# Kernel optimization log

Measured on AMD Instinct MI355X. Metric: run time of the kernel, lower is better.

The kernel has to match this reference:

```python
import jax, jax.numpy as jnp
import numpy as np

INPUT_DIM = 512
KEY_DIM = 256
VOCAB = 10000
MAX_LEN = 300


def setup_inputs() -> dict:
    key = jax.random.key(0)
    ks = jax.random.split(key, 20)
    s = 0.05
    B, S, D, K, V = 32, 196, INPUT_DIM, KEY_DIM, VOCAB
    inp = {
        'x': jax.random.normal(ks[0], (B, S, D), jnp.float32),
        'emb': jax.random.normal(ks[1], (V, D), jnp.float32) * s,
        'Wk': jax.random.normal(ks[2], (K, D), jnp.float32) * s,
        'bk': jnp.zeros((K,), jnp.float32),
        'Wv': jax.random.normal(ks[3], (K, D), jnp.float32) * s,
        'bv': jnp.zeros((K,), jnp.float32),
        'Wq': jax.random.normal(ks[4], (K, D), jnp.float32) * s,
        'bq': jnp.zeros((K,), jnp.float32),
        'Wp': jax.random.normal(ks[5], (V, D + K), jnp.float32) * s,
        'bp': jnp.zeros((V,), jnp.float32),
        # LSTM cell 0: input = concat(embed, context) -> D + K
        'Wih0': jax.random.normal(ks[6], (4 * D, D + K), jnp.float32) * s,
        'Whh0': jax.random.normal(ks[7], (4 * D, D), jnp.float32) * s,
        'bih0': jnp.zeros((4 * D,), jnp.float32),
        'bhh0': jnp.zeros((4 * D,), jnp.float32),
        # LSTM cell 1: input = hidden of cell 0 -> D
        'Wih1': jax.random.normal(ks[8], (4 * D, D), jnp.float32) * s,
        'Whh1': jax.random.normal(ks[9], (4 * D, D), jnp.float32) * s,
        'bih1': jnp.zeros((4 * D,), jnp.float32),
        'bhh1': jnp.zeros((4 * D,), jnp.float32),
    }
    return inp


def _lstm_cell(inp, h, c, Wih, Whh, bih, bhh):
    # torch LSTMCell gate order: i, f, g, o
    gates = inp @ Wih.T + bih + h @ Whh.T + bhh
    i, f, g, o = jnp.split(gates, 4, axis=-1)
    c_new = jax.nn.sigmoid(f) * c + jax.nn.sigmoid(i) * jnp.tanh(g)
    h_new = jax.nn.sigmoid(o) * jnp.tanh(c_new)
    return h_new, c_new


def reference(x, emb, Wk, bk, Wv, bv, Wq, bq, Wp, bp,
              Wih0, Whh0, bih0, bhh0, Wih1, Whh1, bih1, bhh1):
    B = x.shape[0]
    D = Whh0.shape[1]
    K = Wk.shape[0]
    scale = 1.0 / jnp.sqrt(jnp.asarray(K, x.dtype))
    keys = x @ Wk.T + bk      # (B, S, K)
    values = x @ Wv.T + bv    # (B, S, K)

    tok0 = jnp.zeros((B,), jnp.int32)           # argmax of zeros(B,1) == 0
    ctx0 = jnp.zeros((B, K), x.dtype)
    h0 = jnp.zeros((B, D), x.dtype)
    c0 = jnp.zeros((B, D), x.dtype)
    h1 = jnp.zeros((B, D), x.dtype)
    c1 = jnp.zeros((B, D), x.dtype)

    def step(carry, _):
        tok, ctx, h0, c0, h1, c1 = carry
        embed = jnp.concatenate([emb[tok], ctx], axis=1)   # (B, D+K)
        h0, c0 = _lstm_cell(embed, h0, c0, Wih0, Whh0, bih0, bhh0)
        h1, c1 = _lstm_cell(h0, h1, c1, Wih1, Whh1, bih1, bhh1)
        q = h1 @ Wq.T + bq                                  # (B, K)
        energy = jnp.einsum('bsk,bk->bs', keys, q) * scale  # (B, S)
        attn = jax.nn.softmax(energy, axis=-1)
        ctx = jnp.einsum('bs,bsk->bk', attn, values)        # (B, K)
        out = jnp.concatenate([h1, ctx], axis=1)            # (B, D+K)
        pred = out @ Wp.T + bp                              # (B, V)
        tok = jnp.argmax(pred, axis=-1).astype(jnp.int32)
        return (tok, ctx, h0, c0, h1, c1), pred

    _, preds = jax.lax.scan(step, (tok0, ctx0, h0, c0, h1, c1), None, length=MAX_LEN)
    return jnp.transpose(preds, (1, 0, 2))  # (B, MAX_LEN, V)
```

## Files before the change

kernel.cpp:

```cpp
#include <hip/hip_runtime.h>
#include <math.h>


typedef unsigned long long u64;

#define NS 196
#define ND 512
#define NK 256
#define NV 10000
#define NT 300
#define NBLK 256
#define NTHR 512
#define SCOPE __HIP_MEMORY_SCOPE_AGENT

__device__ __forceinline__ float sigm(float x) { return 1.0f / (1.0f + expf(-x)); }

__device__ __forceinline__ float aldf(const float* p) {
  return __hip_atomic_load(p, __ATOMIC_RELAXED, SCOPE);
}
__device__ __forceinline__ void astf(float* p, float v) {
  __hip_atomic_store(p, v, __ATOMIC_RELAXED, SCOPE);
}
__device__ __forceinline__ u64 aldu(const u64* p) {
  return __hip_atomic_load(p, __ATOMIC_RELAXED, SCOPE);
}
__device__ __forceinline__ void astu(u64* p, u64 v) {
  __hip_atomic_store(p, v, __ATOMIC_RELAXED, SCOPE);
}

__device__ __forceinline__ u64 packmax(float x, int v) {
  unsigned u = __float_as_uint(x);
  u = (u & 0x80000000u) ? ~u : (u | 0x80000000u);
  return ((u64)u << 32) | (u64)(0xFFFFFFFFu - (unsigned)v);
}

__device__ __forceinline__ int eslot(int b, int k4) {
  return b * 32 + ((k4 & ~7) | ((k4 ^ b) & 7));
}

__device__ __forceinline__ void gbar(unsigned* bar, int bid, unsigned ep, bool fenced) {
  __syncthreads();
  if (threadIdx.x == 0) {
    if (fenced) __threadfence();
    asm volatile("s_waitcnt vmcnt(0)" ::: "memory");
    const int g = bid & 7;
    const unsigned old = __hip_atomic_fetch_add(&bar[g * 32], 1u, __ATOMIC_RELAXED, SCOPE);
    if (old == ep * 32u - 1u) {
      const unsigned r = __hip_atomic_fetch_add(&bar[512], 1u, __ATOMIC_RELAXED, SCOPE);
      if (r == ep * 8u - 1u) {
#pragma unroll
        for (int i = 0; i < 8; ++i)
          __hip_atomic_store(&bar[256 + i * 32], ep, __ATOMIC_RELAXED, SCOPE);
      }
    }
    while (__hip_atomic_load(&bar[256 + g * 32], __ATOMIC_RELAXED, SCOPE) < ep)
      __builtin_amdgcn_s_sleep(2);
    if (fenced) __threadfence();
  }
  __syncthreads();
}

__global__ __launch_bounds__(256) void k_zbar(unsigned* bar) {
  const int i = blockIdx.x * 256 + threadIdx.x;
  if (i < 1024) bar[i] = 0u;
}

struct Params {
  const float *x, *emb, *Wk, *bk, *Wv, *bv, *Wq, *bq, *Wp, *bp;
  const float *Wih0, *Whh0, *bih0, *bhh0, *Wih1, *Whh1, *bih1, *bhh1;
  float *out, *keys, *values, *h0t, *h1t, *c0, *c1, *ctx, *qg;
  u64 *amax;
  unsigned *bar;
};

__global__ __launch_bounds__(NTHR, 1) void k_all(Params p) {
  extern __shared__ float dyn[];
  float* Wp_lds = dyn;
  float* stage  = dyn + 30720;

  __shared__ __align__(16) float arena[2560];
  __shared__ int tok_lds[32];
  __shared__ u64 cand2[32][10];

  const int bid = blockIdx.x;
  const int t = threadIdx.x;
  const int lane = t & 63;
  const int w = t >> 6;

#define GP(ks, r, b)  arena[((ks) * 8 + (r)) * 32 + (b)]
#define GS(r, b)      arena[1024 + (r) * 32 + (b)]

  {
    const int g = bid * NTHR + t;
    if (g < 65536) astf(&p.h0t[g], 0.0f);
    if (g < 8192) astf(&p.ctx[g], 0.0f);
    if (g < 256) astu(&p.amax[g], (g < 32) ? ((1ull << 32) | 0xFFFFFFFFull) : 0ull);
  }
  if (t < 64) {
    const int idx = (bid * 2 + (t >> 5)) * 32 + (t & 31);
    p.c0[idx] = 0.0f;
    p.c1[idx] = 0.0f;
  }
  if (bid < 250) {
    const float* src = p.Wp + (size_t)bid * 40 * 768;
    for (int i = t; i < 7680; i += NTHR)
      *(float4*)(Wp_lds + 4 * i) = *(const float4*)(src + 4 * i);
  }
  {
    const int kc = bid & 7, bb = bid >> 3;
    const int kl = t & 31, sg = t >> 5;
    const int k = kc * 32 + kl;
    float ak[13], av[13];
#pragma unroll
    for (int i = 0; i < 13; ++i) { ak[i] = 0.f; av[i] = 0.f; }
    const float* wkr = p.Wk + (size_t)k * ND;
    const float* wvr = p.Wv + (size_t)k * ND;
    const float* xb = p.x + (size_t)bb * NS * ND;
    for (int j = 0; j < ND; j += 4) {
      const float4 wk4 = *(const float4*)(wkr + j);
      const float4 wv4 = *(const float4*)(wvr + j);
#pragma unroll
      for (int si = 0; si < 13; ++si) {
        const int s = sg + si * 16;
        if (s < NS) {
          const float4 xv = *(const float4*)(xb + (size_t)s * ND + j);
          ak[si] += wk4.x * xv.x + wk4.y * xv.y + wk4.z * xv.z + wk4.w * xv.w;
          av[si] += wv4.x * xv.x + wv4.y * xv.y + wv4.z * xv.z + wv4.w * xv.w;
        }
      }
    }
    const float bkk = p.bk[k], bvv = p.bv[k];
#pragma unroll
    for (int si = 0; si < 13; ++si) {
      const int s = sg + si * 16;
      if (s < NS) {
        const size_t o = ((size_t)bb * NS + s) * NK + k;
        p.keys[o] = ak[si] + bkk;
        p.values[o] = av[si] + bvv;
      }
    }
  }
  unsigned ep = 1;
  gbar(p.bar, bid, ep++, true);

  for (int step = 0; step < NT; ++step) {
    const int cur = step & 1;
    const float* h0c = p.h0t + cur * 16384;
    float* h0n = p.h0t + (cur ^ 1) * 16384;
    const float* h1c = p.h1t + cur * 16384;
    float* h1n = p.h1t + (cur ^ 1) * 16384;

    if (t < 32) {
      u64 m = aldu(&p.amax[t]);
#pragma unroll
      for (int s2 = 1; s2 < 8; ++s2) { const u64 o = aldu(&p.amax[s2 * 32 + t]); if (o > m) m = o; }
      tok_lds[t] = (int)(0xFFFFFFFFu - (unsigned)(m & 0xFFFFFFFFull));
    }
    __syncthreads();
    {
      const int rq = w >> 2, ks = w & 3;
      const int b = lane & 31, kq = lane >> 5;
      const int s8 = ks * 2 + kq;
      const int rb = rq * 4;
      int rg4[4];
#pragma unroll
      for (int i = 0; i < 4; ++i) rg4[i] = ((rb + i) >> 1) * ND + bid * 2 + ((rb + i) & 1);
      float a0 = 0.f, a1 = 0.f, a2 = 0.f, a3 = 0.f;
      for (int c = 0; c < 4; ++c) {
        {
          const int eb = t >> 4, sl = t & 15;
          const float* er = p.emb + (size_t)tok_lds[eb] * ND + c * 128;
          *(float4*)(stage + 4 * eslot(eb, sl)) = *(const float4*)(er + 4 * sl);
          *(float4*)(stage + 4 * eslot(eb, sl + 16)) = *(const float4*)(er + 4 * (sl + 16));
        }
        __syncthreads();
#pragma unroll
        for (int jj = 0; jj < 4; ++jj) {
          const int f4 = ks * 8 + kq * 4 + jj;
          const float4 a4 = *(const float4*)(stage + 4 * eslot(b, f4));
          const int wc = c * 128 + 4 * f4;
          const float4 q0 = *(const float4*)(p.Wih0 + (size_t)rg4[0] * 768 + wc);
          const float4 q1 = *(const float4*)(p.Wih0 + (size_t)rg4[1] * 768 + wc);
          const float4 q2 = *(const float4*)(p.Wih0 + (size_t)rg4[2] * 768 + wc);
          const float4 q3 = *(const float4*)(p.Wih0 + (size_t)rg4[3] * 768 + wc);
          a0 += q0.x * a4.x + q0.y * a4.y + q0.z * a4.z + q0.w * a4.w;
          a1 += q1.x * a4.x + q1.y * a4.y + q1.z * a4.z + q1.w * a4.w;
          a2 += q2.x * a4.x + q2.y * a4.y + q2.z * a4.z + q2.w * a4.w;
          a3 += q3.x * a4.x + q3.y * a4.y + q3.z * a4.z + q3.w * a4.w;
        }
        __syncthreads();
      }
#pragma unroll 4
      for (int j = 0; j < 8; ++j) {
        const int k0 = (s8 * 8 + j) * 4;
        float4 x4;
        x4.x = aldf(p.ctx + (k0 + 0) * 32 + b);
        x4.y = aldf(p.ctx + (k0 + 1) * 32 + b);
        x4.z = aldf(p.ctx + (k0 + 2) * 32 + b);
        x4.w = aldf(p.ctx + (k0 + 3) * 32 + b);
        const int wc = 512 + k0;
        const float4 q0 = *(const float4*)(p.Wih0 + (size_t)rg4[0] * 768 + wc);
        const float4 q1 = *(const float4*)(p.Wih0 + (size_t)rg4[1] * 768 + wc);
        const float4 q2 = *(const float4*)(p.Wih0 + (size_t)rg4[2] * 768 + wc);
        const float4 q3 = *(const float4*)(p.Wih0 + (size_t)rg4[3] * 768 + wc);
        a0 += q0.x * x4.x + q0.y * x4.y + q0.z * x4.z + q0.w * x4.w;
        a1 += q1.x * x4.x + q1.y * x4.y + q1.z * x4.z + q1.w * x4.w;
        a2 += q2.x * x4.x + q2.y * x4.y + q2.z * x4.z + q2.w * x4.w;
        a3 += q3.x * x4.x + q3.y * x4.y + q3.z * x4.z + q3.w * x4.w;
      }
#pragma unroll 4
      for (int j = 0; j < 16; ++j) {
        const int k0 = (s8 * 16 + j) * 4;
        float4 x4;
        x4.x = aldf(h0c + (k0 + 0) * 32 + b);
        x4.y = aldf(h0c + (k0 + 1) * 32 + b);
        x4.z = aldf(h0c + (k0 + 2) * 32 + b);
        x4.w = aldf(h0c + (k0 + 3) * 32 + b);
        const float4 q0 = *(const float4*)(p.Whh0 + (size_t)rg4[0] * ND + k0);
        const float4 q1 = *(const float4*)(p.Whh0 + (size_t)rg4[1] * ND + k0);
        const float4 q2 = *(const float4*)(p.Whh0 + (size_t)rg4[2] * ND + k0);
        const float4 q3 = *(const float4*)(p.Whh0 + (size_t)rg4[3] * ND + k0);
        a0 += q0.x * x4.x + q0.y * x4.y + q0.z * x4.z + q0.w * x4.w;
        a1 += q1.x * x4.x + q1.y * x4.y + q1.z * x4.z + q1.w * x4.w;
        a2 += q2.x * x4.x + q2.y * x4.y + q2.z * x4.z + q2.w * x4.w;
        a3 += q3.x * x4.x + q3.y * x4.y + q3.z * x4.z + q3.w * x4.w;
      }
      a0 += __shfl_xor(a0, 32);
      a1 += __shfl_xor(a1, 32);
      a2 += __shfl_xor(a2, 32);
      a3 += __shfl_xor(a3, 32);
      if (kq == 0) {
        GP(ks, rb + 0, b) = a0; GP(ks, rb + 1, b) = a1;
        GP(ks, rb + 2, b) = a2; GP(ks, rb + 3, b) = a3;
      }
    }
    __syncthreads();
    if (t < 256) {
      const int r = t >> 5, b2 = t & 31;
      const int grow = (r >> 1) * ND + bid * 2 + (r & 1);
      GS(r, b2) = GP(0, r, b2) + GP(1, r, b2) + GP(2, r, b2) + GP(3, r, b2)
                + p.bih0[grow] + p.bhh0[grow];
    }
    __syncthreads();
    if (t < 64) {
      const int dl = t >> 5, b2 = t & 31;
      const int idx = (bid * 2 + dl) * 32 + b2;
      const float gi = GS(0 + dl, b2), gf = GS(2 + dl, b2);
      const float gg = GS(4 + dl, b2), go = GS(6 + dl, b2);
      const float cn = sigm(gf) * p.c0[idx] + sigm(gi) * tanhf(gg);
      p.c0[idx] = cn;
      astf(&h0n[idx], sigm(go) * tanhf(cn));
    }
    gbar(p.bar, bid, ep++, false);

    if (bid == 0 && t < 256) astu(&p.amax[t], 0ull);
    {
      const int rq = w >> 2, ks = w & 3;
      const int b = lane & 31, kq = lane >> 5;
      const int s8 = ks * 2 + kq;
      int rg4[4];
#pragma unroll
      for (int i = 0; i < 4; ++i) {
        const int lr = rq * 4 + i;
        rg4[i] = (lr >> 1) * ND + bid * 2 + (lr & 1);
      }
      float a0 = 0.f, a1 = 0.f, a2 = 0.f, a3 = 0.f;
#pragma unroll 4
      for (int j = 0; j < 32; ++j) {
        const int k0 = s8 * 128 + j * 4;
        const float* src = (k0 < 512) ? (h0n + k0 * 32) : (h1c + (k0 - 512) * 32);
        float4 x4;
        x4.x = aldf(src + 0 * 32 + b);
        x4.y = aldf(src + 1 * 32 + b);
        x4.z = aldf(src + 2 * 32 + b);
        x4.w = aldf(src + 3 * 32 + b);
        const float* wbase = (k0 < 512) ? (p.Wih1 + k0) : (p.Whh1 + (k0 - 512));
        const float4 q0 = *(const float4*)(wbase + (size_t)rg4[0] * ND);
        const float4 q1 = *(const float4*)(wbase + (size_t)rg4[1] * ND);
        const float4 q2 = *(const float4*)(wbase + (size_t)rg4[2] * ND);
        const float4 q3 = *(const float4*)(wbase + (size_t)rg4[3] * ND);
        a0 += q0.x * x4.x + q0.y * x4.y + q0.z * x4.z + q0.w * x4.w;
        a1 += q1.x * x4.x + q1.y * x4.y + q1.z * x4.z + q1.w * x4.w;
        a2 += q2.x * x4.x + q2.y * x4.y + q2.z * x4.z + q2.w * x4.w;
        a3 += q3.x * x4.x + q3.y * x4.y + q3.z * x4.z + q3.w * x4.w;
      }
      a0 += __shfl_xor(a0, 32);
      a1 += __shfl_xor(a1, 32);
      a2 += __shfl_xor(a2, 32);
      a3 += __shfl_xor(a3, 32);
      if (kq == 0) {
        GP(ks, rq * 4 + 0, b) = a0; GP(ks, rq * 4 + 1, b) = a1;
        GP(ks, rq * 4 + 2, b) = a2; GP(ks, rq * 4 + 3, b) = a3;
      }
    }
    __syncthreads();
    if (t < 256) {
      const int r = t >> 5, b2 = t & 31;
      const int grow = (r >> 1) * ND + bid * 2 + (r & 1);
      GS(r, b2) = GP(0, r, b2) + GP(1, r, b2) + GP(2, r, b2) + GP(3, r, b2)
                + p.bih1[grow] + p.bhh1[grow];
    }
    __syncthreads();
    if (t < 64) {
      const int dl = t >> 5, b2 = t & 31;
      const int idx = (bid * 2 + dl) * 32 + b2;
      const float gi = GS(0 + dl, b2), gf = GS(2 + dl, b2);
      const float gg = GS(4 + dl, b2), go = GS(6 + dl, b2);
      const float cn = sigm(gf) * p.c1[idx] + sigm(gi) * tanhf(gg);
      p.c1[idx] = cn;
      astf(&h1n[idx], sigm(go) * tanhf(cn));
    }
    gbar(p.bar, bid, ep++, false);

    if (bid < 64) {
      const int sl = t >> 5, b = t & 31;
      float acc0 = 0.f, acc1 = 0.f, acc2 = 0.f, acc3 = 0.f;
      const float* wq0 = p.Wq + (size_t)(bid * 4 + 0) * ND + sl * 32;
      const float* wq1 = p.Wq + (size_t)(bid * 4 + 1) * ND + sl * 32;
      const float* wq2 = p.Wq + (size_t)(bid * 4 + 2) * ND + sl * 32;
      const float* wq3 = p.Wq + (size_t)(bid * 4 + 3) * ND + sl * 32;
#pragma unroll 8
      for (int kk = 0; kk < 32; ++kk) {
        const float hv = aldf(h1n + (sl * 32 + kk) * 32 + b);
        acc0 += wq0[kk] * hv; acc1 += wq1[kk] * hv;
        acc2 += wq2[kk] * hv; acc3 += wq3[kk] * hv;
      }
      arena[(sl * 4 + 0) * 32 + b] = acc0;
      arena[(sl * 4 + 1) * 32 + b] = acc1;
      arena[(sl * 4 + 2) * 32 + b] = acc2;
      arena[(sl * 4 + 3) * 32 + b] = acc3;
      __syncthreads();
      if (t < 128) {
        const int rl = t >> 5, b2 = t & 31;
        float q = 0.f;
#pragma unroll
        for (int s2 = 0; s2 < 16; ++s2) q += arena[(s2 * 4 + rl) * 32 + b2];
        const int r = bid * 4 + rl;
        astf(&p.qg[r * 32 + b2], (q + p.bq[r]) * 0.0625f);
      }
    }
    gbar(p.bar, bid, ep++, false);

    if (bid < 32) {
      const int b = bid;
      float* attq = arena;
      float* red = arena + 256;
      float* smx = arena + 512;
      if (t < 256) attq[t] = aldf(&p.qg[t * 32 + b]);
      __syncthreads();
      const int kl = lane & 31, rh = lane >> 5;
      for (int pp = 0; pp < 13; ++pp) {
        const int s = pp * 16 + w * 2 + rh;
        float a = 0.f;
        if (s < NS) {
          const float* kr = p.keys + ((size_t)b * NS + s) * NK + kl * 4;
#pragma unroll
          for (int i = 0; i < 2; ++i) {
            const float4 k4 = *(const float4*)(kr + i * 128);
            const float4 q4 = *(const float4*)(attq + i * 128 + kl * 4);
            a += k4.x * q4.x + k4.y * q4.y + k4.z * q4.z + k4.w * q4.w;
          }
        }
#pragma unroll
        for (int mk = 1; mk < 32; mk <<= 1) a += __shfl_xor(a, mk);
        if (kl == 0 && s < NS) smx[s] = a;
      }
      __syncthreads();
      float e = -INFINITY;
      if (t < 256) { e = (t < NS) ? smx[t] : -INFINITY; red[t] = e; }
      __syncthreads();
      for (int off = 128; off; off >>= 1) {
        if (t < off) red[t] = fmaxf(red[t], red[t + off]);
        __syncthreads();
      }
      const float mx = red[0];
      __syncthreads();
      float a = 0.f;
      if (t < 256) { a = (t < NS) ? expf(e - mx) : 0.f; red[t] = a; }
      __syncthreads();
      for (int off = 128; off; off >>= 1) {
        if (t < off) red[t] += red[t + off];
        __syncthreads();
      }
      const float inv = 1.0f / red[0];
      if (t < 256) smx[t] = a * inv;
      __syncthreads();
      if (t < 256) {
        const float* vb = p.values + (size_t)b * NS * NK + t;
        float c0_ = 0.f, c1_ = 0.f, c2_ = 0.f, c3_ = 0.f;
        for (int s = 0; s < NS; s += 4) {
          c0_ += smx[s + 0] * vb[(size_t)(s + 0) * NK];
          c1_ += smx[s + 1] * vb[(size_t)(s + 1) * NK];
          c2_ += smx[s + 2] * vb[(size_t)(s + 2) * NK];
          c3_ += smx[s + 3] * vb[(size_t)(s + 3) * NK];
        }
        astf(&p.ctx[t * 32 + b], (c0_ + c1_) + (c2_ + c3_));
      }
    }
    gbar(p.bar, bid, ep++, false);

    if (bid < 250) {
      const int rgrp = w >> 1, ks2 = w & 1;
      const int b = lane & 31, kq = lane >> 5;
      const int s4 = ks2 * 2 + kq;
      float acc[10];
#pragma unroll
      for (int r = 0; r < 10; ++r) acc[r] = 0.f;
#pragma unroll 2
      for (int j = 0; j < 48; ++j) {
        const int k0 = (s4 * 48 + j) * 4;
        const float* src = (k0 < 512) ? (h1n + k0 * 32) : (p.ctx + (k0 - 512) * 32);
        float4 x4;
        x4.x = aldf(src + 0 * 32 + b);
        x4.y = aldf(src + 1 * 32 + b);
        x4.z = aldf(src + 2 * 32 + b);
        x4.w = aldf(src + 3 * 32 + b);
#pragma unroll
        for (int r = 0; r < 10; ++r) {
          const float4 w4 = *(const float4*)(Wp_lds + (size_t)(rgrp * 10 + r) * 768 + k0);
          acc[r] += w4.x * x4.x + w4.y * x4.y + w4.z * x4.z + w4.w * x4.w;
        }
      }
#pragma unroll
      for (int r = 0; r < 10; ++r) acc[r] += __shfl_xor(acc[r], 32);
      if (kq == 0) {
#pragma unroll
        for (int r = 0; r < 10; ++r)
          arena[ks2 * 1280 + (rgrp * 10 + r) * 32 + b] = acc[r];
      }
      __syncthreads();
      if (t < 320) {
        const int b2 = t & 31, rg = t >> 5;
        const int vb = bid * 40 + rg * 4;
        float4 v;
        float* vp = &v.x;
#pragma unroll
        for (int i = 0; i < 4; ++i) {
          const int row = rg * 4 + i;
          vp[i] = arena[row * 32 + b2] + arena[1280 + row * 32 + b2] + p.bp[vb + i];
        }
        *(float4*)(p.out + ((size_t)b2 * NT + step) * NV + vb) = v;
        u64 m = packmax(v.x, vb + 0);
        u64 o1 = packmax(v.y, vb + 1); if (o1 > m) m = o1;
        u64 o2 = packmax(v.z, vb + 2); if (o2 > m) m = o2;
        u64 o3 = packmax(v.w, vb + 3); if (o3 > m) m = o3;
        cand2[b2][rg] = m;
      }
      __syncthreads();
      if (t < 32) {
        u64 mm = cand2[t][0];
#pragma unroll
        for (int i = 1; i < 10; ++i) { const u64 o = cand2[t][i]; if (o > mm) mm = o; }
        (void)__hip_atomic_fetch_max(&p.amax[(bid & 7) * 32 + t], mm, __ATOMIC_RELAXED, SCOPE);
      }
    }
    gbar(p.bar, bid, ep++, false);
  }
#undef GP
#undef GS
}

extern "C" void kernel_launch(void* const* d_in, const int* in_sizes, int n_in,
                              void* d_out, int out_size, void* d_ws, size_t ws_size,
                              hipStream_t stream) {
  (void)in_sizes; (void)n_in; (void)out_size; (void)ws_size;
  Params prm;
  prm.x    = (const float*)d_in[0];
  prm.emb  = (const float*)d_in[1];
  prm.Wk   = (const float*)d_in[2];
  prm.bk   = (const float*)d_in[3];
  prm.Wv   = (const float*)d_in[4];
  prm.bv   = (const float*)d_in[5];
  prm.Wq   = (const float*)d_in[6];
  prm.bq   = (const float*)d_in[7];
  prm.Wp   = (const float*)d_in[8];
  prm.bp   = (const float*)d_in[9];
  prm.Wih0 = (const float*)d_in[10];
  prm.Whh0 = (const float*)d_in[11];
  prm.bih0 = (const float*)d_in[12];
  prm.bhh0 = (const float*)d_in[13];
  prm.Wih1 = (const float*)d_in[14];
  prm.Whh1 = (const float*)d_in[15];
  prm.bih1 = (const float*)d_in[16];
  prm.bhh1 = (const float*)d_in[17];
  prm.out  = (float*)d_out;

  float* ws = (float*)d_ws;
  prm.keys   = ws;
  prm.values = prm.keys + 1605632;
  prm.h0t    = prm.values + 1605632;
  prm.h1t    = prm.h0t + 32768;
  prm.c0     = prm.h1t + 32768;
  prm.c1     = prm.c0 + 16384;
  prm.ctx    = prm.c1 + 16384;
  prm.amax   = (u64*)(prm.ctx + 8192);
  prm.qg     = prm.ctx + 8192 + 512;
  prm.bar    = (unsigned*)(prm.qg + 8192);

  const int LDS = (30720 + 4096) * 4;
  (void)hipFuncSetAttribute((const void*)k_all, hipFuncAttributeMaxDynamicSharedMemorySize, LDS);

  k_zbar<<<4, 256, 0, stream>>>(prm.bar);
  void* args[] = { &prm };
  (void)hipLaunchCooperativeKernel((const void*)k_all, dim3(NBLK), dim3(NTHR), args,
                                   (unsigned)LDS, stream);
}
```

Measured before the change: 26.78 ms.

## Keep LSTM weights in LDS, fuse query into attention, overlap prediction with attention

Each block now keeps its slice of the LSTM weights (Wih0/Whh0/Wih1/Whh1) resident in LDS instead of the Wp slice, and reads Wp from global memory. The separate query-projection phase and its grid barrier are removed: the 32 attention blocks compute q themselves. Meanwhile blocks below 209 start the h1 part of the output projection, and only the ctx part waits for the next barrier. This cuts one grid barrier per step and removes the repeated global LSTM weight loads, at the cost of streaming Wp from global or L2 every step. The barrier spin sleep is also shortened.

```diff
diff --git a/kernel.cpp b/kernel.cpp
--- a/kernel.cpp
+++ b/kernel.cpp
@@ -11,6 +11,8 @@
 #define NT 300
 #define NBLK 256
 #define NTHR 512
+#define NPRED 209
+#define ATT0 224
 #define SCOPE __HIP_MEMORY_SCOPE_AGENT
 
 __device__ __forceinline__ float sigm(float x) { return 1.0f / (1.0f + expf(-x)); }
@@ -54,7 +56,7 @@
       }
     }
     while (__hip_atomic_load(&bar[256 + g * 32], __ATOMIC_RELAXED, SCOPE) < ep)
-      __builtin_amdgcn_s_sleep(2);
+      __builtin_amdgcn_s_sleep(1);
     if (fenced) __threadfence();
   }
   __syncthreads();
@@ -68,19 +70,20 @@
 struct Params {
   const float *x, *emb, *Wk, *bk, *Wv, *bv, *Wq, *bq, *Wp, *bp;
   const float *Wih0, *Whh0, *bih0, *bhh0, *Wih1, *Whh1, *bih1, *bhh1;
-  float *out, *keys, *values, *h0t, *h1t, *c0, *c1, *ctx, *qg;
+  float *out, *keys, *values, *h0t, *h1t, *c0, *c1, *ctx;
   u64 *amax;
   unsigned *bar;
 };
 
 __global__ __launch_bounds__(NTHR, 1) void k_all(Params p) {
   extern __shared__ float dyn[];
-  float* Wp_lds = dyn;
-  float* stage  = dyn + 30720;
+  float* W0lds = dyn;
+  float* W1lds = dyn + 10240;
+  float* stage = dyn + 18432;
 
   __shared__ __align__(16) float arena[2560];
   __shared__ int tok_lds[32];
-  __shared__ u64 cand2[32][10];
+  __shared__ u64 cand2[32][12];
 
   const int bid = blockIdx.x;
   const int t = threadIdx.x;
@@ -101,10 +104,27 @@
     p.c0[idx] = 0.0f;
     p.c1[idx] = 0.0f;
   }
-  if (bid < 250) {
-    const float* src = p.Wp + (size_t)bid * 40 * 768;
-    for (int i = t; i < 7680; i += NTHR)
-      *(float4*)(Wp_lds + 4 * i) = *(const float4*)(src + 4 * i);
+  {
+    const int r = t >> 6, ln = t & 63;
+    const int grow = (r >> 1) * ND + bid * 2 + (r & 1);
+    const float* s0i = p.Wih0 + (size_t)grow * 768;
+    const float* s0h = p.Whh0 + (size_t)grow * ND;
+#pragma unroll
+    for (int j = 0; j < 5; ++j) {
+      const int col = 4 * (ln + 64 * j);
+      const float4 v = (col < 768) ? *(const float4*)(s0i + col)
+                                   : *(const float4*)(s0h + (col - 768));
+      *(float4*)(W0lds + r * 1280 + col) = v;
+    }
+    const float* s1i = p.Wih1 + (size_t)grow * ND;
+    const float* s1h = p.Whh1 + (size_t)grow * ND;
+#pragma unroll
+    for (int j = 0; j < 4; ++j) {
+      const int col = 4 * (ln + 64 * j);
+      const float4 v = (col < 512) ? *(const float4*)(s1i + col)
+                                   : *(const float4*)(s1h + (col - 512));
+      *(float4*)(W1lds + r * 1024 + col) = v;
+    }
   }
   {
     const int kc = bid & 7, bb = bid >> 3;
@@ -162,9 +182,6 @@
       const int b = lane & 31, kq = lane >> 5;
       const int s8 = ks * 2 + kq;
       const int rb = rq * 4;
-      int rg4[4];
-#pragma unroll
-      for (int i = 0; i < 4; ++i) rg4[i] = ((rb + i) >> 1) * ND + bid * 2 + ((rb + i) & 1);
       float a0 = 0.f, a1 = 0.f, a2 = 0.f, a3 = 0.f;
       for (int c = 0; c < 4; ++c) {
         {
@@ -179,10 +196,10 @@
           const int f4 = ks * 8 + kq * 4 + jj;
           const float4 a4 = *(const float4*)(stage + 4 * eslot(b, f4));
           const int wc = c * 128 + 4 * f4;
-          const float4 q0 = *(const float4*)(p.Wih0 + (size_t)rg4[0] * 768 + wc);
-          const float4 q1 = *(const float4*)(p.Wih0 + (size_t)rg4[1] * 768 + wc);
-          const float4 q2 = *(const float4*)(p.Wih0 + (size_t)rg4[2] * 768 + wc);
-          const float4 q3 = *(const float4*)(p.Wih0 + (size_t)rg4[3] * 768 + wc);
+          const float4 q0 = *(const float4*)(W0lds + (rb + 0) * 1280 + wc);
+          const float4 q1 = *(const float4*)(W0lds + (rb + 1) * 1280 + wc);
+          const float4 q2 = *(const float4*)(W0lds + (rb + 2) * 1280 + wc);
+          const float4 q3 = *(const float4*)(W0lds + (rb + 3) * 1280 + wc);
           a0 += q0.x * a4.x + q0.y * a4.y + q0.z * a4.z + q0.w * a4.w;
           a1 += q1.x * a4.x + q1.y * a4.y + q1.z * a4.z + q1.w * a4.w;
           a2 += q2.x * a4.x + q2.y * a4.y + q2.z * a4.z + q2.w * a4.w;
@@ -199,10 +216,10 @@
         x4.z = aldf(p.ctx + (k0 + 2) * 32 + b);
         x4.w = aldf(p.ctx + (k0 + 3) * 32 + b);
         const int wc = 512 + k0;
-        const float4 q0 = *(const float4*)(p.Wih0 + (size_t)rg4[0] * 768 + wc);
-        const float4 q1 = *(const float4*)(p.Wih0 + (size_t)rg4[1] * 768 + wc);
-        const float4 q2 = *(const float4*)(p.Wih0 + (size_t)rg4[2] * 768 + wc);
-        const float4 q3 = *(const float4*)(p.Wih0 + (size_t)rg4[3] * 768 + wc);
+        const float4 q0 = *(const float4*)(W0lds + (rb + 0) * 1280 + wc);
+        const float4 q1 = *(const float4*)(W0lds + (rb + 1) * 1280 + wc);
+        const float4 q2 = *(const float4*)(W0lds + (rb + 2) * 1280 + wc);
+        const float4 q3 = *(const float4*)(W0lds + (rb + 3) * 1280 + wc);
         a0 += q0.x * x4.x + q0.y * x4.y + q0.z * x4.z + q0.w * x4.w;
         a1 += q1.x * x4.x + q1.y * x4.y + q1.z * x4.z + q1.w * x4.w;
         a2 += q2.x * x4.x + q2.y * x4.y + q2.z * x4.z + q2.w * x4.w;
@@ -216,10 +233,11 @@
         x4.y = aldf(h0c + (k0 + 1) * 32 + b);
         x4.z = aldf(h0c + (k0 + 2) * 32 + b);
         x4.w = aldf(h0c + (k0 + 3) * 32 + b);
-        const float4 q0 = *(const float4*)(p.Whh0 + (size_t)rg4[0] * ND + k0);
-        const float4 q1 = *(const float4*)(p.Whh0 + (size_t)rg4[1] * ND + k0);
-        const float4 q2 = *(const float4*)(p.Whh0 + (size_t)rg4[2] * ND + k0);
-        const float4 q3 = *(const float4*)(p.Whh0 + (size_t)rg4[3] * ND + k0);
+        const int wc = 768 + k0;
+        const float4 q0 = *(const float4*)(W0lds + (rb + 0) * 1280 + wc);
+        const float4 q1 = *(const float4*)(W0lds + (rb + 1) * 1280 + wc);
+        const float4 q2 = *(const float4*)(W0lds + (rb + 2) * 1280 + wc);
+        const float4 q3 = *(const float4*)(W0lds + (rb + 3) * 1280 + wc);
         a0 += q0.x * x4.x + q0.y * x4.y + q0.z * x4.z + q0.w * x4.w;
         a1 += q1.x * x4.x + q1.y * x4.y + q1.z * x4.z + q1.w * x4.w;
         a2 += q2.x * x4.x + q2.y * x4.y + q2.z * x4.z + q2.w * x4.w;
@@ -258,12 +276,7 @@
       const int rq = w >> 2, ks = w & 3;
       const int b = lane & 31, kq = lane >> 5;
       const int s8 = ks * 2 + kq;
-      int rg4[4];
-#pragma unroll
-      for (int i = 0; i < 4; ++i) {
-        const int lr = rq * 4 + i;
-        rg4[i] = (lr >> 1) * ND + bid * 2 + (lr & 1);
-      }
+      const int rb = rq * 4;
       float a0 = 0.f, a1 = 0.f, a2 = 0.f, a3 = 0.f;
 #pragma unroll 4
       for (int j = 0; j < 32; ++j) {
@@ -274,11 +287,10 @@
         x4.y = aldf(src + 1 * 32 + b);
         x4.z = aldf(src + 2 * 32 + b);
         x4.w = aldf(src + 3 * 32 + b);
-        const float* wbase = (k0 < 512) ? (p.Wih1 + k0) : (p.Whh1 + (k0 - 512));
-        const float4 q0 = *(const float4*)(wbase + (size_t)rg4[0] * ND);
-        const float4 q1 = *(const float4*)(wbase + (size_t)rg4[1] * ND);
-        const float4 q2 = *(const float4*)(wbase + (size_t)rg4[2] * ND);
-        const float4 q3 = *(const float4*)(wbase + (size_t)rg4[3] * ND);
+        const float4 q0 = *(const float4*)(W1lds + (rb + 0) * 1024 + k0);
+        const float4 q1 = *(const float4*)(W1lds + (rb + 1) * 1024 + k0);
+        const float4 q2 = *(const float4*)(W1lds + (rb + 2) * 1024 + k0);
+        const float4 q3 = *(const float4*)(W1lds + (rb + 3) * 1024 + k0);
         a0 += q0.x * x4.x + q0.y * x4.y + q0.z * x4.z + q0.w * x4.w;
         a1 += q1.x * x4.x + q1.y * x4.y + q1.z * x4.z + q1.w * x4.w;
         a2 += q2.x * x4.x + q2.y * x4.y + q2.z * x4.z + q2.w * x4.w;
@@ -289,8 +301,8 @@
       a2 += __shfl_xor(a2, 32);
       a3 += __shfl_xor(a3, 32);
       if (kq == 0) {
-        GP(ks, rq * 4 + 0, b) = a0; GP(ks, rq * 4 + 1, b) = a1;
-        GP(ks, rq * 4 + 2, b) = a2; GP(ks, rq * 4 + 3, b) = a3;
+        GP(ks, rb + 0, b) = a0; GP(ks, rb + 1, b) = a1;
+        GP(ks, rb + 2, b) = a2; GP(ks, rb + 3, b) = a3;
       }
     }
     __syncthreads();
@@ -312,43 +324,33 @@
     }
     gbar(p.bar, bid, ep++, false);
 
-    if (bid < 64) {
-      const int sl = t >> 5, b = t & 31;
-      float acc0 = 0.f, acc1 = 0.f, acc2 = 0.f, acc3 = 0.f;
-      const float* wq0 = p.Wq + (size_t)(bid * 4 + 0) * ND + sl * 32;
-      const float* wq1 = p.Wq + (size_t)(bid * 4 + 1) * ND + sl * 32;
-      const float* wq2 = p.Wq + (size_t)(bid * 4 + 2) * ND + sl * 32;
-      const float* wq3 = p.Wq + (size_t)(bid * 4 + 3) * ND + sl * 32;
-#pragma unroll 8
-      for (int kk = 0; kk < 32; ++kk) {
-        const float hv = aldf(h1n + (sl * 32 + kk) * 32 + b);
-        acc0 += wq0[kk] * hv; acc1 += wq1[kk] * hv;
-        acc2 += wq2[kk] * hv; acc3 += wq3[kk] * hv;
-      }
-      arena[(sl * 4 + 0) * 32 + b] = acc0;
-      arena[(sl * 4 + 1) * 32 + b] = acc1;
-      arena[(sl * 4 + 2) * 32 + b] = acc2;
-      arena[(sl * 4 + 3) * 32 + b] = acc3;
-      __syncthreads();
-      if (t < 128) {
-        const int rl = t >> 5, b2 = t & 31;
-        float q = 0.f;
-#pragma unroll
-        for (int s2 = 0; s2 < 16; ++s2) q += arena[(s2 * 4 + rl) * 32 + b2];
-        const int r = bid * 4 + rl;
-        astf(&p.qg[r * 32 + b2], (q + p.bq[r]) * 0.0625f);
-      }
-    }
-    gbar(p.bar, bid, ep++, false);
-
-    if (bid < 32) {
-      const int b = bid;
-      float* attq = arena;
-      float* red = arena + 256;
-      float* smx = arena + 512;
-      if (t < 256) attq[t] = aldf(&p.qg[t * 32 + b]);
+    float acc[6];
+#pragma unroll
+    for (int r = 0; r < 6; ++r) acc[r] = 0.f;
+    if (bid >= ATT0) {
+      const int b = bid - ATT0;
+      float* hb  = arena;
+      float* qs  = arena + 512;
+      float* red = arena + 768;
+      float* smx = arena + 1024;
+      hb[t] = aldf(h1n + t * 32 + b);
       __syncthreads();
       const int kl = lane & 31, rh = lane >> 5;
+      for (int pp = 0; pp < 16; ++pp) {
+        const int r = w * 32 + pp * 2 + rh;
+        const float* wq = p.Wq + (size_t)r * ND + kl * 4;
+        float a = 0.f;
+#pragma unroll
+        for (int i = 0; i < 4; ++i) {
+          const float4 w4 = *(const float4*)(wq + i * 128);
+          const float4 h4 = *(const float4*)(hb + i * 128 + kl * 4);
+          a += w4.x * h4.x + w4.y * h4.y + w4.z * h4.z + w4.w * h4.w;
+        }
+#pragma unroll
+        for (int mk = 1; mk < 32; mk <<= 1) a += __shfl_xor(a, mk);
+        if (kl == 0) qs[r] = (a + p.bq[r]) * 0.0625f;
+      }
+      __syncthreads();
       for (int pp = 0; pp < 13; ++pp) {
         const int s = pp * 16 + w * 2 + rh;
         float a = 0.f;
@@ -357,7 +359,7 @@
 #pragma unroll
           for (int i = 0; i < 2; ++i) {
             const float4 k4 = *(const float4*)(kr + i * 128);
-            const float4 q4 = *(const float4*)(attq + i * 128 + kl * 4);
+            const float4 q4 = *(const float4*)(qs + i * 128 + kl * 4);
             a += k4.x * q4.x + k4.y * q4.y + k4.z * q4.z + k4.w * q4.w;
           }
         }
@@ -396,61 +398,82 @@
         }
         astf(&p.ctx[t * 32 + b], (c0_ + c1_) + (c2_ + c3_));
       }
+    } else if (bid < NPRED) {
+      const int b = lane & 31, kq = lane >> 5;
+      const int rbase = bid * 48 + w * 6;
+      int rc[6];
+#pragma unroll
+      for (int r = 0; r < 6; ++r) rc[r] = (rbase + r < NV) ? (rbase + r) : (NV - 1);
+#pragma unroll 2
+      for (int j = 0; j < 64; ++j) {
+        const int k0 = kq * 256 + j * 4;
+        float4 x4;
+        x4.x = aldf(h1n + (k0 + 0) * 32 + b);
+        x4.y = aldf(h1n + (k0 + 1) * 32 + b);
+        x4.z = aldf(h1n + (k0 + 2) * 32 + b);
+        x4.w = aldf(h1n + (k0 + 3) * 32 + b);
+#pragma unroll
+        for (int r = 0; r < 6; ++r) {
+          const float4 w4 = *(const float4*)(p.Wp + (size_t)rc[r] * 768 + k0);
+          acc[r] += w4.x * x4.x + w4.y * x4.y + w4.z * x4.z + w4.w * x4.w;
+        }
+      }
     }
     gbar(p.bar, bid, ep++, false);
 
-    if (bid < 250) {
-      const int rgrp = w >> 1, ks2 = w & 1;
+    if (bid < NPRED) {
       const int b = lane & 31, kq = lane >> 5;
-      const int s4 = ks2 * 2 + kq;
-      float acc[10];
-#pragma unroll
-      for (int r = 0; r < 10; ++r) acc[r] = 0.f;
+      const int rbase = bid * 48 + w * 6;
+      int rc[6];
+#pragma unroll
+      for (int r = 0; r < 6; ++r) rc[r] = (rbase + r < NV) ? (rbase + r) : (NV - 1);
 #pragma unroll 2
-      for (int j = 0; j < 48; ++j) {
-        const int k0 = (s4 * 48 + j) * 4;
-        const float* src = (k0 < 512) ? (h1n + k0 * 32) : (p.ctx + (k0 - 512) * 32);
+      for (int j = 0; j < 32; ++j) {
+        const int kc_ = kq * 128 + j * 4;
         float4 x4;
-        x4.x = aldf(src + 0 * 32 + b);
-        x4.y = aldf(src + 1 * 32 + b);
-        x4.z = aldf(src + 2 * 32 + b);
-        x4.w = aldf(src + 3 * 32 + b);
-#pragma unroll
-        for (int r = 0; r < 10; ++r) {
-          const float4 w4 = *(const float4*)(Wp_lds + (size_t)(rgrp * 10 + r) * 768 + k0);
+        x4.x = aldf(p.ctx + (kc_ + 0) * 32 + b);
+        x4.y = aldf(p.ctx + (kc_ + 1) * 32 + b);
+        x4.z = aldf(p.ctx + (kc_ + 2) * 32 + b);
+        x4.w = aldf(p.ctx + (kc_ + 3) * 32 + b);
+#pragma unroll
+        for (int r = 0; r < 6; ++r) {
+          const float4 w4 = *(const float4*)(p.Wp + (size_t)rc[r] * 768 + 512 + kc_);
           acc[r] += w4.x * x4.x + w4.y * x4.y + w4.z * x4.z + w4.w * x4.w;
         }
       }
 #pragma unroll
-      for (int r = 0; r < 10; ++r) acc[r] += __shfl_xor(acc[r], 32);
+      for (int r = 0; r < 6; ++r) acc[r] += __shfl_xor(acc[r], 32);
       if (kq == 0) {
 #pragma unroll
-        for (int r = 0; r < 10; ++r)
-          arena[ks2 * 1280 + (rgrp * 10 + r) * 32 + b] = acc[r];
-      }
-      __syncthreads();
-      if (t < 320) {
+        for (int r = 0; r < 6; ++r)
+          arena[(w * 6 + r) * 32 + b] = acc[r];
+      }
+      __syncthreads();
+      if (t < 384) {
         const int b2 = t & 31, rg = t >> 5;
-        const int vb = bid * 40 + rg * 4;
-        float4 v;
-        float* vp = &v.x;
-#pragma unroll
-        for (int i = 0; i < 4; ++i) {
-          const int row = rg * 4 + i;
-          vp[i] = arena[row * 32 + b2] + arena[1280 + row * 32 + b2] + p.bp[vb + i];
-        }
-        *(float4*)(p.out + ((size_t)b2 * NT + step) * NV + vb) = v;
-        u64 m = packmax(v.x, vb + 0);
-        u64 o1 = packmax(v.y, vb + 1); if (o1 > m) m = o1;
-        u64 o2 = packmax(v.z, vb + 2); if (o2 > m) m = o2;
-        u64 o3 = packmax(v.w, vb + 3); if (o3 > m) m = o3;
+        const int vb = bid * 48 + rg * 4;
+        u64 m = 0ull;
+        if (vb + 3 < NV) {
+          float4 v;
+          float* vp = &v.x;
+#pragma unroll
+          for (int i = 0; i < 4; ++i) {
+            const int row = rg * 4 + i;
+            vp[i] = arena[row * 32 + b2] + p.bp[vb + i];
+          }
+          *(float4*)(p.out + ((size_t)b2 * NT + step) * NV + vb) = v;
+          m = packmax(v.x, vb + 0);
+          const u64 o1 = packmax(v.y, vb + 1); if (o1 > m) m = o1;
+          const u64 o2 = packmax(v.z, vb + 2); if (o2 > m) m = o2;
+          const u64 o3 = packmax(v.w, vb + 3); if (o3 > m) m = o3;
+        }
         cand2[b2][rg] = m;
       }
       __syncthreads();
       if (t < 32) {
         u64 mm = cand2[t][0];
 #pragma unroll
-        for (int i = 1; i < 10; ++i) { const u64 o = cand2[t][i]; if (o > mm) mm = o; }
+        for (int i = 1; i < 12; ++i) { const u64 o = cand2[t][i]; if (o > mm) mm = o; }
         (void)__hip_atomic_fetch_max(&p.amax[(bid & 7) * 32 + t], mm, __ATOMIC_RELAXED, SCOPE);
       }
     }
@@ -494,10 +517,9 @@
   prm.c1     = prm.c0 + 16384;
   prm.ctx    = prm.c1 + 16384;
   prm.amax   = (u64*)(prm.ctx + 8192);
-  prm.qg     = prm.ctx + 8192 + 512;
-  prm.bar    = (unsigned*)(prm.qg + 8192);
-
-  const int LDS = (30720 + 4096) * 4;
+  prm.bar    = (unsigned*)(prm.amax + 256);
+
+  const int LDS = (10240 + 8192 + 4096) * 4;
   (void)hipFuncSetAttribute((const void*)k_all, hipFuncAttributeMaxDynamicSharedMemorySize, LDS);
 
   k_zbar<<<4, 256, 0, stream>>>(prm.bar);
```

New measurement: 24.84 ms. 7.3% less time.
